# Kernel tuning notes

Measured on AMD Instinct MI355X. Metric: run time of the kernel, lower is better.

The kernel has to match this reference:

```python
import jax, jax.numpy as jnp
import numpy as np

B, S, DM = 2, 2048, 1024
H, HD = 16, 64          # n_heads, head_dim
TPF = 128               # tokens_per_frame
NF = S // TPF           # n_frames
EPS = 1e-6
ROPE_THETA = 10000.0
NEG = -1e30  # stand-in for -inf that stays finite under softmax


def setup_inputs() -> dict:
    key = jax.random.key(0)
    ks = jax.random.split(key, 3)
    x = jax.random.normal(ks[0], (B, S, DM), dtype=jnp.float32)
    Wqkv = jax.random.normal(ks[1], (3 * DM, DM), dtype=jnp.float32) * (DM ** -0.5)
    bqkv = jnp.zeros((3 * DM,), dtype=jnp.float32)
    Wout = jax.random.normal(ks[2], (DM, DM), dtype=jnp.float32) * (DM ** -0.5)
    bout = jnp.zeros((DM,), dtype=jnp.float32)
    q_scale = jnp.ones((HD,), dtype=jnp.float32)
    k_scale = jnp.ones((HD,), dtype=jnp.float32)
    return {"x": x, "Wqkv": Wqkv, "bqkv": bqkv, "q_scale": q_scale,
            "k_scale": k_scale, "Wout": Wout, "bout": bout}


def _block_causal_mask(dtype):
    # Frame-block causal: query in frame i may attend keys in frames <= i.
    # Quirk from source: rows of the LAST frame additionally mask frame 0.
    fr = jnp.arange(S) // TPF
    allowed = fr[None, :] <= fr[:, None]
    quirk = (fr[:, None] == NF - 1) & (fr[None, :] == 0)
    allowed = allowed & ~quirk
    return jnp.where(allowed, jnp.zeros((), dtype), jnp.full((), NEG, dtype))


def _rmsnorm(t, scale):
    return t * jax.lax.rsqrt(jnp.mean(t * t, axis=-1, keepdims=True) + EPS) * scale


def _rope(t):
    # half-split rotary over flat token index; t: [B,H,S,D]
    pos = jnp.arange(S, dtype=jnp.float32)
    inv_freq = 1.0 / (ROPE_THETA ** (jnp.arange(0, HD, 2, dtype=jnp.float32) / HD))
    ang = pos[:, None] * inv_freq[None, :]              # [S, D/2]
    cos = jnp.concatenate([jnp.cos(ang), jnp.cos(ang)], axis=-1)  # [S, D]
    sin = jnp.concatenate([jnp.sin(ang), jnp.sin(ang)], axis=-1)
    t1, t2 = jnp.split(t, 2, axis=-1)
    rot = jnp.concatenate([-t2, t1], axis=-1)
    return t * cos + rot * sin


def reference(x, Wqkv, bqkv, q_scale, k_scale, Wout, bout):
    qkv = x @ Wqkv.T + bqkv                        # [B,S,3*DM]
    qkv = qkv.reshape(B, S, 3, H, HD)
    q, k, v = jnp.moveaxis(qkv, 2, 0)              # each [B,S,H,D]
    q = jnp.transpose(q, (0, 2, 1, 3))             # [B,H,S,D]
    k = jnp.transpose(k, (0, 2, 1, 3))
    v = jnp.transpose(v, (0, 2, 1, 3))
    q = _rmsnorm(q, q_scale)
    k = _rmsnorm(k, k_scale)
    q = _rope(q)
    k = _rope(k)
    mask = _block_causal_mask(x.dtype)             # [S,S]
    scores = jnp.einsum('bhqd,bhkd->bhqk', q, k) * (HD ** -0.5) + mask
    attn = jax.nn.softmax(scores, axis=-1)
    o = jnp.einsum('bhqk,bhkd->bhqd', attn, v)     # [B,H,S,D]
    o = jnp.transpose(o, (0, 2, 1, 3)).reshape(B, S, DM)
    return o @ Wout.T + bout
```

## Files before the change

kernel.cpp:

```cpp
#include <hip/hip_runtime.h>
#include <cstddef>
#include <cstdint>

constexpr int CB  = 2;
constexpr int CS  = 2048;
constexpr int CDM = 1024;
constexpr int CH  = 16;
constexpr int CHD = 64;
constexpr int CTPF = 128;
constexpr int CNF = 16;

typedef __attribute__((ext_vector_type(8))) short short8;
typedef __attribute__((ext_vector_type(4))) float f32x4;

__device__ inline ushort f32_bf16_rne(float x) {
  uint32_t u = __float_as_uint(x);
  u += 0x7FFFu + ((u >> 16) & 1u);
  return (ushort)(u >> 16);
}
__device__ inline float bf16_f32(ushort h) {
  return __uint_as_float(((uint32_t)h) << 16);
}
__device__ inline void split8(const float* v, short8& H, short8& L) {
#pragma unroll
  for (int j = 0; j < 8; ++j) {
    const ushort hh = f32_bf16_rne(v[j]);
    H[j] = (short)hh;
    L[j] = (short)f32_bf16_rne(v[j] - bf16_f32(hh));
  }
}

__global__ __launch_bounds__(256) void split_pass(
    const float* __restrict__ src, ushort* __restrict__ h,
    ushort* __restrict__ l, int n8) {
  int i = blockIdx.x * 256 + threadIdx.x;
  const int stride = gridDim.x * 256;
  for (; i < n8; i += stride) {
    float v[8];
    *(float4*)&v[0] = ((const float4*)src)[2 * i];
    *(float4*)&v[4] = ((const float4*)src)[2 * i + 1];
    short8 H, L;
    split8(v, H, L);
    *(short8*)&h[(size_t)i * 8] = H;
    *(short8*)&l[(size_t)i * 8] = L;
  }
}

__global__ __launch_bounds__(256) void gemm_ps(
    const ushort* __restrict__ Ah, const ushort* __restrict__ Al,
    const ushort* __restrict__ Bh, const ushort* __restrict__ Bl,
    const float* __restrict__ bias, float* __restrict__ C,
    int M, int N, int K) {
  __shared__ ushort As_h[128 * 32], As_l[128 * 32];
  __shared__ ushort Bs_h[128 * 32], Bs_l[128 * 32];
  const int tid = threadIdx.x;
  const int bm = blockIdx.y * 128;
  const int bn = blockIdx.x * 128;
  const int wid = tid >> 6;
  const int lane = tid & 63;
  const int wm = wid >> 1;
  const int wn = wid & 1;
  const int l15 = lane & 15;
  const int lk = lane >> 4;
  const int srow = tid >> 2;
  const int kq = (tid & 3) * 8;

  f32x4 acc[4][4];
#pragma unroll
  for (int i = 0; i < 4; ++i)
#pragma unroll
    for (int j = 0; j < 4; ++j) acc[i][j] = (f32x4){0.f, 0.f, 0.f, 0.f};

  for (int k0 = 0; k0 < K; k0 += 32) {
    __syncthreads();
#pragma unroll
    for (int c = 0; c < 2; ++c) {
      const int row = srow + c * 64;
      const int kg = kq ^ ((row & 6) << 2);
      const size_t ga = (size_t)(bm + row) * K + k0 + kg;
      const size_t gb = (size_t)(bn + row) * K + k0 + kg;
      const int lo = tid * 8 + c * 2048;
      __builtin_amdgcn_global_load_lds(
          (const __attribute__((address_space(1))) void*)(Ah + ga),
          (__attribute__((address_space(3))) void*)&As_h[lo], 16, 0, 0);
      __builtin_amdgcn_global_load_lds(
          (const __attribute__((address_space(1))) void*)(Al + ga),
          (__attribute__((address_space(3))) void*)&As_l[lo], 16, 0, 0);
      __builtin_amdgcn_global_load_lds(
          (const __attribute__((address_space(1))) void*)(Bh + gb),
          (__attribute__((address_space(3))) void*)&Bs_h[lo], 16, 0, 0);
      __builtin_amdgcn_global_load_lds(
          (const __attribute__((address_space(1))) void*)(Bl + gb),
          (__attribute__((address_space(3))) void*)&Bs_l[lo], 16, 0, 0);
    }
    __syncthreads();

    short8 ah[4], al[4], bh[4], bl[4];
#pragma unroll
    for (int fI = 0; fI < 4; ++fI) {
      const int ar = wm * 64 + fI * 16 + l15;
      const int aoff = ar * 32 + ((lk * 8) ^ ((ar & 6) << 2));
      ah[fI] = *(const short8*)&As_h[aoff];
      al[fI] = *(const short8*)&As_l[aoff];
      const int br = wn * 64 + fI * 16 + l15;
      const int boff = br * 32 + ((lk * 8) ^ ((br & 6) << 2));
      bh[fI] = *(const short8*)&Bs_h[boff];
      bl[fI] = *(const short8*)&Bs_l[boff];
    }
#pragma unroll
    for (int mf = 0; mf < 4; ++mf)
#pragma unroll
      for (int nf = 0; nf < 4; ++nf) {
        acc[mf][nf] = __builtin_amdgcn_mfma_f32_16x16x32_bf16(
            ah[mf], bh[nf], acc[mf][nf], 0, 0, 0);
        acc[mf][nf] = __builtin_amdgcn_mfma_f32_16x16x32_bf16(
            ah[mf], bl[nf], acc[mf][nf], 0, 0, 0);
        acc[mf][nf] = __builtin_amdgcn_mfma_f32_16x16x32_bf16(
            al[mf], bh[nf], acc[mf][nf], 0, 0, 0);
      }
  }

#pragma unroll
  for (int mf = 0; mf < 4; ++mf)
#pragma unroll
    for (int nf = 0; nf < 4; ++nf) {
      const int col = bn + wn * 64 + nf * 16 + l15;
      const int row0 = bm + wm * 64 + mf * 16 + lk * 4;
      const float bc = bias[col];
#pragma unroll
      for (int i = 0; i < 4; ++i)
        C[(size_t)(row0 + i) * N + col] = acc[mf][nf][i] + bc;
    }
}

__global__ __launch_bounds__(256) void qkv_prep(
    const float* __restrict__ qkv, const float* __restrict__ q_scale,
    const float* __restrict__ k_scale,
    ushort* __restrict__ Qh, ushort* __restrict__ Ql,
    ushort* __restrict__ Kh, ushort* __restrict__ Kl,
    ushort* __restrict__ Vth, ushort* __restrict__ Vtl) {
  __shared__ float Vtile[64][68];
  const int lane = threadIdx.x & 63;
  const int w = threadIdx.x >> 6;
  const int st = blockIdx.x;
  const int h = blockIdx.y;
  const int b = blockIdx.z;

  const float qs = q_scale[lane];
  const float ks = k_scale[lane];
  const int j = lane & 31;
  const float inv = powf(10000.0f, -(float)j * (1.0f / 32.0f));
  const float sgn = (lane < 32) ? -1.f : 1.f;

  for (int it = 0; it < 16; ++it) {
    const int sl = w * 16 + it;
    const int s = st * 64 + sl;
    const size_t row =
        ((size_t)(b * CS + s)) * (3 * CDM) + (size_t)h * CHD + lane;
    float qv = qkv[row];
    float kv = qkv[row + CDM];
    const float vv = qkv[row + 2 * CDM];

    float sq = qv * qv, sk2 = kv * kv;
#pragma unroll
    for (int off = 32; off > 0; off >>= 1) {
      sq += __shfl_xor(sq, off);
      sk2 += __shfl_xor(sk2, off);
    }
    qv *= rsqrtf(sq * (1.f / CHD) + 1e-6f) * qs;
    kv *= rsqrtf(sk2 * (1.f / CHD) + 1e-6f) * ks;

    const float ang = (float)s * inv;
    const float cs = cosf(ang);
    const float sn = sinf(ang);
    const float qp = __shfl_xor(qv, 32);
    const float kp = __shfl_xor(kv, 32);
    const float qr = fmaf(qv, cs, sgn * qp * sn) * 0.125f;
    const float kr = fmaf(kv, cs, sgn * kp * sn);

    const size_t ob = (((size_t)(b * CH + h)) * CS + s) * CHD + lane;
    const ushort qhh = f32_bf16_rne(qr);
    Qh[ob] = qhh;
    Ql[ob] = f32_bf16_rne(qr - bf16_f32(qhh));
    const ushort khh = f32_bf16_rne(kr);
    Kh[ob] = khh;
    Kl[ob] = f32_bf16_rne(kr - bf16_f32(khh));
    Vtile[lane][sl] = vv;
  }
  __syncthreads();
  const int d = threadIdx.x >> 2;
  const int sq4 = (threadIdx.x & 3) * 16;
  const size_t vb = (((size_t)(b * CH + h)) * CHD + d) * CS + st * 64 + sq4;
#pragma unroll
  for (int j0 = 0; j0 < 16; j0 += 8) {
    float v8[8];
#pragma unroll
    for (int jj = 0; jj < 8; ++jj) v8[jj] = Vtile[d][sq4 + j0 + jj];
    short8 H, L;
    split8(v8, H, L);
    *(short8*)&Vth[vb + j0] = H;
    *(short8*)&Vtl[vb + j0] = L;
  }
}

__global__ __launch_bounds__(256, 2) void attn_fwd_mfma(
    const ushort* __restrict__ Qh, const ushort* __restrict__ Ql,
    const ushort* __restrict__ Kh, const ushort* __restrict__ Kl,
    const ushort* __restrict__ Vth, const ushort* __restrict__ Vtl,
    ushort* __restrict__ Oh, ushort* __restrict__ Ol) {
  __shared__ ushort Ks_h[64 * 64], Ks_l[64 * 64];
  __shared__ ushort Vs_h[64 * 64], Vs_l[64 * 64];
  __shared__ ushort Ps_h[128 * 64], Ps_l[128 * 64];
  const int tid = threadIdx.x;
  const int b = blockIdx.x;
  const int h = blockIdx.y;
  const int fsel = blockIdx.z;
  const int f = (fsel < 8) ? (15 - fsel) : (fsel - 8);
  const int lane = tid & 63;
  const int wid = tid >> 6;
  const int l15 = lane & 15;
  const int lk = lane >> 4;
  const int qb = wid * 32;
  const size_t hb = ((size_t)(b * CH + h)) * CS * CHD;
  const size_t vtb = ((size_t)(b * CH + h)) * CHD * CS;

  short8 qh[2][2], ql[2][2];
#pragma unroll
  for (int nf = 0; nf < 2; ++nf)
#pragma unroll
    for (int ks = 0; ks < 2; ++ks) {
      const size_t qoff = hb +
          (size_t)(f * CTPF + qb + nf * 16 + l15) * CHD + ks * 32 + lk * 8;
      qh[nf][ks] = *(const short8*)(Qh + qoff);
      ql[nf][ks] = *(const short8*)(Ql + qoff);
    }

  f32x4 accO[2][4];
#pragma unroll
  for (int mo = 0; mo < 2; ++mo)
#pragma unroll
    for (int no = 0; no < 4; ++no) accO[mo][no] = (f32x4){0.f, 0.f, 0.f, 0.f};
  float m[2] = {-1e30f, -1e30f};
  float lsum[2] = {0.f, 0.f};

  const int kf0 = (f == CNF - 1) ? 1 : 0;
  for (int kf = kf0; kf <= f; ++kf) {
#pragma unroll 1
    for (int half = 0; half < 2; ++half) {
      const int cb = kf * CTPF + half * 64;
      __syncthreads();
      {
        const int r = tid >> 2;
        const int cq = (tid & 3) * 16;
        const int mk = (r & 7) << 3;
        const size_t ko = hb + (size_t)(cb + r) * CHD + cq;
        *(short8*)&Ks_h[r * 64 + (cq ^ mk)] = *(const short8*)(Kh + ko);
        *(short8*)&Ks_h[r * 64 + ((cq + 8) ^ mk)] = *(const short8*)(Kh + ko + 8);
        *(short8*)&Ks_l[r * 64 + (cq ^ mk)] = *(const short8*)(Kl + ko);
        *(short8*)&Ks_l[r * 64 + ((cq + 8) ^ mk)] = *(const short8*)(Kl + ko + 8);
        const size_t vo = vtb + (size_t)r * CS + cb + cq;
        *(short8*)&Vs_h[r * 64 + (cq ^ mk)] = *(const short8*)(Vth + vo);
        *(short8*)&Vs_h[r * 64 + ((cq + 8) ^ mk)] = *(const short8*)(Vth + vo + 8);
        *(short8*)&Vs_l[r * 64 + (cq ^ mk)] = *(const short8*)(Vtl + vo);
        *(short8*)&Vs_l[r * 64 + ((cq + 8) ^ mk)] = *(const short8*)(Vtl + vo + 8);
      }
      __syncthreads();

      f32x4 sacc[4][2];
#pragma unroll
      for (int mf = 0; mf < 4; ++mf)
#pragma unroll
        for (int nf = 0; nf < 2; ++nf) sacc[mf][nf] = (f32x4){0.f, 0.f, 0.f, 0.f};
#pragma unroll
      for (int ks = 0; ks < 2; ++ks) {
        short8 kh[4], kl[4];
#pragma unroll
        for (int mf = 0; mf < 4; ++mf) {
          const int krow = mf * 16 + l15;
          const int base = krow * 64 + ((ks * 32 + lk * 8) ^ ((krow & 7) << 3));
          kh[mf] = *(const short8*)&Ks_h[base];
          kl[mf] = *(const short8*)&Ks_l[base];
        }
#pragma unroll
        for (int mf = 0; mf < 4; ++mf)
#pragma unroll
          for (int nf = 0; nf < 2; ++nf) {
            sacc[mf][nf] = __builtin_amdgcn_mfma_f32_16x16x32_bf16(
                kh[mf], qh[nf][ks], sacc[mf][nf], 0, 0, 0);
            sacc[mf][nf] = __builtin_amdgcn_mfma_f32_16x16x32_bf16(
                kh[mf], ql[nf][ks], sacc[mf][nf], 0, 0, 0);
            sacc[mf][nf] = __builtin_amdgcn_mfma_f32_16x16x32_bf16(
                kl[mf], qh[nf][ks], sacc[mf][nf], 0, 0, 0);
          }
      }

      float c[2];
#pragma unroll
      for (int nf = 0; nf < 2; ++nf) {
        float cm = sacc[0][nf][0];
#pragma unroll
        for (int mf = 0; mf < 4; ++mf)
#pragma unroll
          for (int i = 0; i < 4; ++i) cm = fmaxf(cm, sacc[mf][nf][i]);
        cm = fmaxf(cm, __shfl_xor(cm, 16));
        cm = fmaxf(cm, __shfl_xor(cm, 32));
        const float mn = fmaxf(m[nf], cm);
        c[nf] = __expf(m[nf] - mn);
        m[nf] = mn;
        float ps = 0.f;
        const int qrow = qb + nf * 16 + l15;
        const int qmk = (qrow & 7) << 3;
#pragma unroll
        for (int mf = 0; mf < 4; ++mf) {
          float p0 = __expf(sacc[mf][nf][0] - mn);
          float p1 = __expf(sacc[mf][nf][1] - mn);
          float p2 = __expf(sacc[mf][nf][2] - mn);
          float p3 = __expf(sacc[mf][nf][3] - mn);
          ps += (p0 + p1) + (p2 + p3);
          const ushort h0 = f32_bf16_rne(p0), h1 = f32_bf16_rne(p1);
          const ushort h2 = f32_bf16_rne(p2), h3 = f32_bf16_rne(p3);
          uint2 hw, lw;
          hw.x = (uint32_t)h0 | ((uint32_t)h1 << 16);
          hw.y = (uint32_t)h2 | ((uint32_t)h3 << 16);
          lw.x = (uint32_t)f32_bf16_rne(p0 - bf16_f32(h0)) |
                 ((uint32_t)f32_bf16_rne(p1 - bf16_f32(h1)) << 16);
          lw.y = (uint32_t)f32_bf16_rne(p2 - bf16_f32(h2)) |
                 ((uint32_t)f32_bf16_rne(p3 - bf16_f32(h3)) << 16);
          const int off = qrow * 64 + ((mf * 16 + lk * 4) ^ qmk);
          *(uint2*)&Ps_h[off] = hw;
          *(uint2*)&Ps_l[off] = lw;
        }
        ps += __shfl_xor(ps, 16);
        ps += __shfl_xor(ps, 32);
        lsum[nf] = lsum[nf] * c[nf] + ps;
      }
#pragma unroll
      for (int mo = 0; mo < 2; ++mo)
#pragma unroll
        for (int i = 0; i < 4; ++i) {
          const float cq = __shfl(c[mo], lk * 4 + i);
#pragma unroll
          for (int no = 0; no < 4; ++no) accO[mo][no][i] *= cq;
        }

#pragma unroll
      for (int ks = 0; ks < 2; ++ks) {
        short8 pa_h[2], pa_l[2], vb_h[4], vb_l[4];
#pragma unroll
        for (int mo = 0; mo < 2; ++mo) {
          const int qrow = qb + mo * 16 + l15;
          const int base = qrow * 64 + ((ks * 32 + lk * 8) ^ ((qrow & 7) << 3));
          pa_h[mo] = *(const short8*)&Ps_h[base];
          pa_l[mo] = *(const short8*)&Ps_l[base];
        }
#pragma unroll
        for (int no = 0; no < 4; ++no) {
          const int vrow = no * 16 + l15;
          const int base = vrow * 64 + ((ks * 32 + lk * 8) ^ ((vrow & 7) << 3));
          vb_h[no] = *(const short8*)&Vs_h[base];
          vb_l[no] = *(const short8*)&Vs_l[base];
        }
#pragma unroll
        for (int mo = 0; mo < 2; ++mo)
#pragma unroll
          for (int no = 0; no < 4; ++no) {
            accO[mo][no] = __builtin_amdgcn_mfma_f32_16x16x32_bf16(
                pa_h[mo], vb_h[no], accO[mo][no], 0, 0, 0);
            accO[mo][no] = __builtin_amdgcn_mfma_f32_16x16x32_bf16(
                pa_h[mo], vb_l[no], accO[mo][no], 0, 0, 0);
            accO[mo][no] = __builtin_amdgcn_mfma_f32_16x16x32_bf16(
                pa_l[mo], vb_h[no], accO[mo][no], 0, 0, 0);
          }
      }
    }
  }

  const float il0 = 1.f / lsum[0];
  const float il1 = 1.f / lsum[1];
#pragma unroll
  for (int mo = 0; mo < 2; ++mo) {
    const float myil = (mo == 0) ? il0 : il1;
#pragma unroll
    for (int i = 0; i < 4; ++i) {
      const float wv = __shfl(myil, lk * 4 + i);
      const int srow = f * CTPF + qb + mo * 16 + lk * 4 + i;
      const size_t obase = (size_t)(b * CS + srow) * CDM + h * CHD;
#pragma unroll
      for (int no = 0; no < 4; ++no) {
        const float val = accO[mo][no][i] * wv;
        const ushort hh = f32_bf16_rne(val);
        Oh[obase + no * 16 + l15] = hh;
        Ol[obase + no * 16 + l15] = f32_bf16_rne(val - bf16_f32(hh));
      }
    }
  }
}

extern "C" void kernel_launch(void* const* d_in, const int* in_sizes, int n_in,
                              void* d_out, int out_size, void* d_ws, size_t ws_size,
                              hipStream_t stream) {
  const float* x       = (const float*)d_in[0];
  const float* Wqkv    = (const float*)d_in[1];
  const float* bqkv    = (const float*)d_in[2];
  const float* q_scale = (const float*)d_in[3];
  const float* k_scale = (const float*)d_in[4];
  const float* Wout    = (const float*)d_in[5];
  const float* bout    = (const float*)d_in[6];
  float* out = (float*)d_out;

  ushort* W = (ushort*)d_ws;
  const size_t qkvN = (size_t)(CB * CS) * (3 * CDM);
  const size_t perA = (size_t)CB * CH * CS * CHD;
  const size_t WqN  = (size_t)(3 * CDM) * CDM;
  const size_t WoN  = (size_t)CDM * CDM;

  float*  qkvF = (float*)W;
  ushort* Oh   = W;
  ushort* Ol   = W + perA;
  ushort* R1   = W + 2 * qkvN;
  ushort* Qh = R1;            ushort* Ql = R1 + perA;
  ushort* Kh = R1 + 2 * perA; ushort* Kl = R1 + 3 * perA;
  ushort* Vth = R1 + 4 * perA; ushort* Vtl = R1 + 5 * perA;
  ushort* xh  = R1;            ushort* xl  = R1 + perA;
  ushort* Wqh = R1 + 2 * perA; ushort* Wql = Wqh + WqN;
  ushort* Wouth = R1 + 6 * perA; ushort* Woutl = Wouth + WoN;

  split_pass<<<2048, 256, 0, stream>>>(x, xh, xl, (int)(perA / 8));
  split_pass<<<1536, 256, 0, stream>>>(Wqkv, Wqh, Wql, (int)(WqN / 8));
  split_pass<<<512, 256, 0, stream>>>(Wout, Wouth, Woutl, (int)(WoN / 8));

  dim3 g1((3 * CDM) / 128, (CB * CS) / 128);
  gemm_ps<<<g1, 256, 0, stream>>>(xh, xl, Wqh, Wql, bqkv, qkvF,
                                  CB * CS, 3 * CDM, CDM);

  dim3 g2(CS / 64, CH, CB);
  qkv_prep<<<g2, 256, 0, stream>>>(qkvF, q_scale, k_scale,
                                   Qh, Ql, Kh, Kl, Vth, Vtl);

  dim3 g3(CB, CH, CNF);
  attn_fwd_mfma<<<g3, 256, 0, stream>>>(Qh, Ql, Kh, Kl, Vth, Vtl, Oh, Ol);

  dim3 g4(CDM / 128, (CB * CS) / 128);
  gemm_ps<<<g4, 256, 0, stream>>>(Oh, Ol, Wouth, Woutl, bout, out,
                                  CB * CS, CDM, CDM);
}
```

Baseline: 256.0 us.

## Fuse RMSNorm, RoPE, bf16 split and V transpose into QKV GEMM epilogue

Replaces the QKV GEMM plus separate qkv_prep kernel with a single GEMM whose epilogue applies bias, RMSNorm across the 64-wide head (shuffle reduction over 16 lanes), rotary embedding, and hi/lo bf16 splitting, writing Q/K directly. V tiles are transposed through shared memory and written as Vt hi/lo. This removes the fp32 qkv intermediate round trip (about 48MB write+read) and one launch, at the cost of a heavier epilogue with scattered 2-byte stores and extra syncs for the V path. The workspace layout is reorganised to match.

```diff
diff --git a/kernel.cpp b/kernel.cpp
--- a/kernel.cpp
+++ b/kernel.cpp
@@ -43,6 +43,184 @@
     split8(v, H, L);
     *(short8*)&h[(size_t)i * 8] = H;
     *(short8*)&l[(size_t)i * 8] = L;
+  }
+}
+
+__global__ __launch_bounds__(256) void gemm_fused_qkv(
+    const ushort* __restrict__ Ah, const ushort* __restrict__ Al,
+    const ushort* __restrict__ Bh, const ushort* __restrict__ Bl,
+    const float* __restrict__ bias, const float* __restrict__ q_scale,
+    const float* __restrict__ k_scale,
+    ushort* __restrict__ Qh, ushort* __restrict__ Ql,
+    ushort* __restrict__ Kh, ushort* __restrict__ Kl,
+    ushort* __restrict__ Vth, ushort* __restrict__ Vtl) {
+  __shared__ ushort As_h[128 * 32], As_l[128 * 32];
+  __shared__ ushort Bs_h[128 * 32], Bs_l[128 * 32];
+  __shared__ ushort VT[64 * 132];
+  const int K = CDM;
+  const int tid = threadIdx.x;
+  const int bnr = blockIdx.x;
+  const int bm = blockIdx.y * 128;
+  const int bn = bnr * 128;
+  const int wid = tid >> 6;
+  const int lane = tid & 63;
+  const int wm = wid >> 1;
+  const int wn = wid & 1;
+  const int l15 = lane & 15;
+  const int lk = lane >> 4;
+  const int srow = tid >> 2;
+  const int kq = (tid & 3) * 8;
+
+  f32x4 acc[4][4];
+#pragma unroll
+  for (int i = 0; i < 4; ++i)
+#pragma unroll
+    for (int j = 0; j < 4; ++j) acc[i][j] = (f32x4){0.f, 0.f, 0.f, 0.f};
+
+  for (int k0 = 0; k0 < K; k0 += 32) {
+    __syncthreads();
+#pragma unroll
+    for (int c = 0; c < 2; ++c) {
+      const int row = srow + c * 64;
+      const int kg = kq ^ ((row & 6) << 2);
+      const size_t ga = (size_t)(bm + row) * K + k0 + kg;
+      const size_t gb = (size_t)(bn + row) * K + k0 + kg;
+      const int lo = tid * 8 + c * 2048;
+      __builtin_amdgcn_global_load_lds(
+          (const __attribute__((address_space(1))) void*)(Ah + ga),
+          (__attribute__((address_space(3))) void*)&As_h[lo], 16, 0, 0);
+      __builtin_amdgcn_global_load_lds(
+          (const __attribute__((address_space(1))) void*)(Al + ga),
+          (__attribute__((address_space(3))) void*)&As_l[lo], 16, 0, 0);
+      __builtin_amdgcn_global_load_lds(
+          (const __attribute__((address_space(1))) void*)(Bh + gb),
+          (__attribute__((address_space(3))) void*)&Bs_h[lo], 16, 0, 0);
+      __builtin_amdgcn_global_load_lds(
+          (const __attribute__((address_space(1))) void*)(Bl + gb),
+          (__attribute__((address_space(3))) void*)&Bs_l[lo], 16, 0, 0);
+    }
+    __syncthreads();
+
+    short8 ah[4], al[4], bh[4], bl[4];
+#pragma unroll
+    for (int fI = 0; fI < 4; ++fI) {
+      const int ar = wm * 64 + fI * 16 + l15;
+      const int aoff = ar * 32 + ((lk * 8) ^ ((ar & 6) << 2));
+      ah[fI] = *(const short8*)&As_h[aoff];
+      al[fI] = *(const short8*)&As_l[aoff];
+      const int br = wn * 64 + fI * 16 + l15;
+      const int boff = br * 32 + ((lk * 8) ^ ((br & 6) << 2));
+      bh[fI] = *(const short8*)&Bs_h[boff];
+      bl[fI] = *(const short8*)&Bs_l[boff];
+    }
+#pragma unroll
+    for (int mf = 0; mf < 4; ++mf)
+#pragma unroll
+      for (int nf = 0; nf < 4; ++nf) {
+        acc[mf][nf] = __builtin_amdgcn_mfma_f32_16x16x32_bf16(
+            ah[mf], bh[nf], acc[mf][nf], 0, 0, 0);
+        acc[mf][nf] = __builtin_amdgcn_mfma_f32_16x16x32_bf16(
+            ah[mf], bl[nf], acc[mf][nf], 0, 0, 0);
+        acc[mf][nf] = __builtin_amdgcn_mfma_f32_16x16x32_bf16(
+            al[mf], bh[nf], acc[mf][nf], 0, 0, 0);
+      }
+  }
+
+#pragma unroll
+  for (int nf = 0; nf < 4; ++nf) {
+    const float bc = bias[bn + wn * 64 + nf * 16 + l15];
+#pragma unroll
+    for (int mf = 0; mf < 4; ++mf)
+#pragma unroll
+      for (int i = 0; i < 4; ++i) acc[mf][nf][i] += bc;
+  }
+
+  const int region = bnr >> 3;
+  const int bloc = bm >> 11;
+  const int sbase = bm & (CS - 1);
+
+  if (region < 2) {
+    const float* scale = (region == 0) ? q_scale : k_scale;
+    ushort* Dh = (region == 0) ? Qh : Kh;
+    ushort* Dl = (region == 0) ? Ql : Kl;
+    const float qmul = (region == 0) ? 0.125f : 1.0f;
+    const int hh = (bnr - region * 8) * 2 + wn;
+    const size_t hbout = ((size_t)(bloc * CH + hh)) * CS;
+    float sc[4];
+#pragma unroll
+    for (int nf = 0; nf < 4; ++nf) sc[nf] = scale[nf * 16 + l15];
+    const float inv0 = powf(10000.0f, -(float)l15 * (1.0f / 32.0f));
+    const float inv1 = powf(10000.0f, -(float)(16 + l15) * (1.0f / 32.0f));
+#pragma unroll
+    for (int mf = 0; mf < 4; ++mf)
+#pragma unroll
+      for (int i = 0; i < 4; ++i) {
+        const int stok = sbase + wm * 64 + mf * 16 + lk * 4 + i;
+        float ss = 0.f;
+#pragma unroll
+        for (int nf = 0; nf < 4; ++nf)
+          ss = fmaf(acc[mf][nf][i], acc[mf][nf][i], ss);
+        ss += __shfl_xor(ss, 1);
+        ss += __shfl_xor(ss, 2);
+        ss += __shfl_xor(ss, 4);
+        ss += __shfl_xor(ss, 8);
+        const float rms = rsqrtf(ss * (1.0f / 64.0f) + 1e-6f);
+        const float v0 = acc[mf][0][i] * rms * sc[0];
+        const float v1 = acc[mf][1][i] * rms * sc[1];
+        const float v2 = acc[mf][2][i] * rms * sc[2];
+        const float v3 = acc[mf][3][i] * rms * sc[3];
+        const float a0 = (float)stok * inv0;
+        const float a1 = (float)stok * inv1;
+        const float c0 = cosf(a0), s0 = sinf(a0);
+        const float c1 = cosf(a1), s1 = sinf(a1);
+        const float o0 = (v0 * c0 - v2 * s0) * qmul;
+        const float o1 = (v1 * c1 - v3 * s1) * qmul;
+        const float o2 = (v2 * c0 + v0 * s0) * qmul;
+        const float o3 = (v3 * c1 + v1 * s1) * qmul;
+        const size_t ob = (hbout + stok) * CHD + l15;
+        ushort t;
+        t = f32_bf16_rne(o0); Dh[ob] = t;
+        Dl[ob] = f32_bf16_rne(o0 - bf16_f32(t));
+        t = f32_bf16_rne(o1); Dh[ob + 16] = t;
+        Dl[ob + 16] = f32_bf16_rne(o1 - bf16_f32(t));
+        t = f32_bf16_rne(o2); Dh[ob + 32] = t;
+        Dl[ob + 32] = f32_bf16_rne(o2 - bf16_f32(t));
+        t = f32_bf16_rne(o3); Dh[ob + 48] = t;
+        Dl[ob + 48] = f32_bf16_rne(o3 - bf16_f32(t));
+      }
+  } else {
+    const int p0 = bnr - 16;
+#pragma unroll 1
+    for (int p = 0; p < 2; ++p) {
+#pragma unroll 1
+      for (int ph = 0; ph < 2; ++ph) {
+        __syncthreads();
+        if (wn == p) {
+#pragma unroll
+          for (int mf = 0; mf < 4; ++mf)
+#pragma unroll
+            for (int nf = 0; nf < 4; ++nf)
+#pragma unroll
+              for (int i = 0; i < 4; ++i) {
+                const float v = acc[mf][nf][i];
+                const ushort hv = f32_bf16_rne(v);
+                const ushort u =
+                    (ph == 0) ? hv : f32_bf16_rne(v - bf16_f32(hv));
+                VT[(nf * 16 + l15) * 132 + wm * 64 + mf * 16 + lk * 4 + i] = u;
+              }
+        }
+        __syncthreads();
+        const int cl = tid >> 2;
+        const int seg = (tid & 3) * 32;
+        const int head = p0 * 2 + p;
+        ushort* dst = ((ph == 0) ? Vth : Vtl) +
+            (((size_t)(bloc * CH + head)) * CHD + cl) * CS + sbase + seg;
+        const ushort* srcp = &VT[cl * 132 + seg];
+#pragma unroll
+        for (int k2 = 0; k2 < 4; ++k2)
+          *(short8*)(dst + k2 * 8) = *(const short8*)(srcp + k2 * 8);
+      }
+    }
   }
 }
 
@@ -131,76 +309,6 @@
       for (int i = 0; i < 4; ++i)
         C[(size_t)(row0 + i) * N + col] = acc[mf][nf][i] + bc;
     }
-}
-
-__global__ __launch_bounds__(256) void qkv_prep(
-    const float* __restrict__ qkv, const float* __restrict__ q_scale,
-    const float* __restrict__ k_scale,
-    ushort* __restrict__ Qh, ushort* __restrict__ Ql,
-    ushort* __restrict__ Kh, ushort* __restrict__ Kl,
-    ushort* __restrict__ Vth, ushort* __restrict__ Vtl) {
-  __shared__ float Vtile[64][68];
-  const int lane = threadIdx.x & 63;
-  const int w = threadIdx.x >> 6;
-  const int st = blockIdx.x;
-  const int h = blockIdx.y;
-  const int b = blockIdx.z;
-
-  const float qs = q_scale[lane];
-  const float ks = k_scale[lane];
-  const int j = lane & 31;
-  const float inv = powf(10000.0f, -(float)j * (1.0f / 32.0f));
-  const float sgn = (lane < 32) ? -1.f : 1.f;
-
-  for (int it = 0; it < 16; ++it) {
-    const int sl = w * 16 + it;
-    const int s = st * 64 + sl;
-    const size_t row =
-        ((size_t)(b * CS + s)) * (3 * CDM) + (size_t)h * CHD + lane;
-    float qv = qkv[row];
-    float kv = qkv[row + CDM];
-    const float vv = qkv[row + 2 * CDM];
-
-    float sq = qv * qv, sk2 = kv * kv;
-#pragma unroll
-    for (int off = 32; off > 0; off >>= 1) {
-      sq += __shfl_xor(sq, off);
-      sk2 += __shfl_xor(sk2, off);
-    }
-    qv *= rsqrtf(sq * (1.f / CHD) + 1e-6f) * qs;
-    kv *= rsqrtf(sk2 * (1.f / CHD) + 1e-6f) * ks;
-
-    const float ang = (float)s * inv;
-    const float cs = cosf(ang);
-    const float sn = sinf(ang);
-    const float qp = __shfl_xor(qv, 32);
-    const float kp = __shfl_xor(kv, 32);
-    const float qr = fmaf(qv, cs, sgn * qp * sn) * 0.125f;
-    const float kr = fmaf(kv, cs, sgn * kp * sn);
-
-    const size_t ob = (((size_t)(b * CH + h)) * CS + s) * CHD + lane;
-    const ushort qhh = f32_bf16_rne(qr);
-    Qh[ob] = qhh;
-    Ql[ob] = f32_bf16_rne(qr - bf16_f32(qhh));
-    const ushort khh = f32_bf16_rne(kr);
-    Kh[ob] = khh;
-    Kl[ob] = f32_bf16_rne(kr - bf16_f32(khh));
-    Vtile[lane][sl] = vv;
-  }
-  __syncthreads();
-  const int d = threadIdx.x >> 2;
-  const int sq4 = (threadIdx.x & 3) * 16;
-  const size_t vb = (((size_t)(b * CH + h)) * CHD + d) * CS + st * 64 + sq4;
-#pragma unroll
-  for (int j0 = 0; j0 < 16; j0 += 8) {
-    float v8[8];
-#pragma unroll
-    for (int jj = 0; jj < 8; ++jj) v8[jj] = Vtile[d][sq4 + j0 + jj];
-    short8 H, L;
-    split8(v8, H, L);
-    *(short8*)&Vth[vb + j0] = H;
-    *(short8*)&Vtl[vb + j0] = L;
-  }
 }
 
 __global__ __launch_bounds__(256, 2) void attn_fwd_mfma(
@@ -409,33 +517,33 @@
   float* out = (float*)d_out;
 
   ushort* W = (ushort*)d_ws;
-  const size_t qkvN = (size_t)(CB * CS) * (3 * CDM);
   const size_t perA = (size_t)CB * CH * CS * CHD;
   const size_t WqN  = (size_t)(3 * CDM) * CDM;
   const size_t WoN  = (size_t)CDM * CDM;
 
-  float*  qkvF = (float*)W;
-  ushort* Oh   = W;
-  ushort* Ol   = W + perA;
-  ushort* R1   = W + 2 * qkvN;
-  ushort* Qh = R1;            ushort* Ql = R1 + perA;
-  ushort* Kh = R1 + 2 * perA; ushort* Kl = R1 + 3 * perA;
-  ushort* Vth = R1 + 4 * perA; ushort* Vtl = R1 + 5 * perA;
-  ushort* xh  = R1;            ushort* xl  = R1 + perA;
-  ushort* Wqh = R1 + 2 * perA; ushort* Wql = Wqh + WqN;
-  ushort* Wouth = R1 + 6 * perA; ushort* Woutl = Wouth + WoN;
+  ushort* Qh  = W;
+  ushort* Ql  = W + perA;
+  ushort* Kh  = W + 2 * perA;
+  ushort* Kl  = W + 3 * perA;
+  ushort* Vth = W + 4 * perA;
+  ushort* Vtl = W + 5 * perA;
+  ushort* xh  = W + 6 * perA;
+  ushort* xl  = W + 7 * perA;
+  ushort* Oh  = xh;
+  ushort* Ol  = xl;
+  ushort* Wqh = W + 8 * perA;
+  ushort* Wql = Wqh + WqN;
+  ushort* Wouth = Wql + WqN;
+  ushort* Woutl = Wouth + WoN;
 
   split_pass<<<2048, 256, 0, stream>>>(x, xh, xl, (int)(perA / 8));
   split_pass<<<1536, 256, 0, stream>>>(Wqkv, Wqh, Wql, (int)(WqN / 8));
   split_pass<<<512, 256, 0, stream>>>(Wout, Wouth, Woutl, (int)(WoN / 8));
 
   dim3 g1((3 * CDM) / 128, (CB * CS) / 128);
-  gemm_ps<<<g1, 256, 0, stream>>>(xh, xl, Wqh, Wql, bqkv, qkvF,
-                                  CB * CS, 3 * CDM, CDM);
-
-  dim3 g2(CS / 64, CH, CB);
-  qkv_prep<<<g2, 256, 0, stream>>>(qkvF, q_scale, k_scale,
-                                   Qh, Ql, Kh, Kl, Vth, Vtl);
+  gemm_fused_qkv<<<g1, 256, 0, stream>>>(xh, xl, Wqh, Wql, bqkv,
+                                         q_scale, k_scale,
+                                         Qh, Ql, Kh, Kl, Vth, Vtl);
 
   dim3 g3(CB, CH, CNF);
   attn_fwd_mfma<<<g3, 256, 0, stream>>>(Qh, Ql, Kh, Kl, Vth, Vtl, Oh, Ol);
```

After: 468.9 us. 1.83x slower.
